# Kernel optimization log

Measured on AMD Instinct MI355X. Metric: run time of the kernel, lower is better.

## Reference

```python
import jax, jax.numpy as jnp
import numpy as np
from jax import lax

H = 512  # LSTM hidden size per direction


def lstm_dir(x, mask, Wih, Whh, bias, reverse):
    # x: [B,L,D], mask: [B,L] float. Masked update follows VarMaskedFastLSTM:
    # state = state_prev + (state_new - state_prev) * mask[t]
    B = x.shape[0]
    h0 = jnp.zeros((B, H), x.dtype)
    c0 = jnp.zeros((B, H), x.dtype)
    xs = jnp.swapaxes(x, 0, 1)      # [L,B,D]
    ms = jnp.swapaxes(mask, 0, 1)   # [L,B]
    if reverse:
        xs, ms = xs[::-1], ms[::-1]
    gx = jnp.einsum('lbd,gd->lbg', xs, Wih) + bias  # precompute input projection [L,B,4H]

    def step(carry, inp):
        h, c = carry
        g_in, mt = inp
        gates = g_in + h @ Whh.T
        i, f, g, o = jnp.split(gates, 4, axis=-1)  # torch gate order i,f,g,o
        c_new = jax.nn.sigmoid(f) * c + jax.nn.sigmoid(i) * jnp.tanh(g)
        h_new = jax.nn.sigmoid(o) * jnp.tanh(c_new)
        m = mt[:, None]
        h = h + (h_new - h) * m
        c = c + (c_new - c) * m
        return (h, c), h

    _, hs = lax.scan(step, (h0, c0), (gx, ms))
    if reverse:
        hs = hs[::-1]
    return jnp.swapaxes(hs, 0, 1)  # [B,L,H]


def bilstm(x, mask, w_ih0, w_hh0, b0, w_ih, w_hh, b):
    out = jnp.concatenate([
        lstm_dir(x, mask, w_ih0[0], w_hh0[0], b0[0], False),
        lstm_dir(x, mask, w_ih0[1], w_hh0[1], b0[1], True)], axis=-1)
    for l in range(2):  # layers 1,2 take 2H-dim input
        out = jnp.concatenate([
            lstm_dir(out, mask, w_ih[l, 0], w_hh[l, 0], b[l, 0], False),
            lstm_dir(out, mask, w_ih[l, 1], w_hh[l, 1], b[l, 1], True)], axis=-1)
    return out  # [B,L,2H]


def setup_inputs() -> dict:
    key = jax.random.key(0)
    ks = jax.random.split(key, 16)
    B, L = 32, 128
    Vin, Vout, E = 32000, 32000, 128
    s = 0.04  # ~1/sqrt(H) init scale
    inp = {}
    inp['inp_word'] = jax.random.randint(ks[0], (B, L), 0, Vin)
    inp['inp_mask'] = jnp.ones((B, L), jnp.float32)
    inp['pri_mask'] = jax.random.randint(ks[1], (B, L), 0, 2).astype(bool)
    inp['tgt_word'] = jax.random.randint(ks[2], (B, L), 0, Vout)
    inp['emb'] = jax.random.normal(ks[3], (Vin, E), jnp.float32) * s
    inp['w_ih0'] = jax.random.normal(ks[4], (2, 4 * H, E), jnp.float32) * s
    inp['w_hh0'] = jax.random.normal(ks[5], (2, 4 * H, H), jnp.float32) * s
    inp['b0'] = jax.random.normal(ks[6], (2, 4 * H), jnp.float32) * s
    inp['w_ih'] = jax.random.normal(ks[7], (2, 2, 4 * H, 2 * H), jnp.float32) * s
    inp['w_hh'] = jax.random.normal(ks[8], (2, 2, 4 * H, H), jnp.float32) * s
    inp['b'] = jax.random.normal(ks[9], (2, 2, 4 * H), jnp.float32) * s
    inp['dec_w1'] = jax.random.normal(ks[10], (128, 2 * H), jnp.float32) * s
    inp['dec_b1'] = jnp.zeros((128,), jnp.float32)
    inp['dec_w2'] = jax.random.normal(ks[11], (Vout, 128), jnp.float32) * s
    inp['dec_b2'] = jnp.zeros((Vout,), jnp.float32)
    inp['ce_weight'] = jax.random.uniform(ks[12], (Vout,), jnp.float32, 0.5, 1.5)
    return inp


def reference(inp_word, inp_mask, pri_mask, tgt_word, emb, w_ih0, w_hh0, b0,
              w_ih, w_hh, b, dec_w1, dec_b1, dec_w2, dec_b2, ce_weight):
    x = emb[inp_word]  # [B,L,E]; inp_drop is identity in eval mode
    seq = bilstm(x, inp_mask, w_ih0, w_hh0, b0, w_ih, w_hh, b)  # [B,L,1024]
    hid = jax.nn.relu(jnp.einsum('blh,dh->bld', seq, dec_w1) + dec_b1)
    decoded = jax.nn.log_softmax(jnp.einsum('bld,vd->blv', hid, dec_w2) + dec_b2, axis=-1)
    rcv_word = jnp.argmax(decoded, axis=-1)
    # Faithful to original: F.cross_entropy applies log_softmax again on the
    # already log-softmaxed decoder output, with class weights (weighted mean).
    lp = jax.nn.log_softmax(decoded, axis=-1)
    B, L, V = lp.shape
    lp = lp.reshape(B * L, V)
    tgt = tgt_word.reshape(-1)
    w = ce_weight[tgt]
    nll = -jnp.take_along_axis(lp, tgt[:, None], axis=1)[:, 0]
    loss = jnp.sum(nll * w) / jnp.sum(w)
    return loss, rcv_word
```

## Files before the change

### kernel.cpp

```cpp
#include <hip/hip_runtime.h>
#include <math.h>

#define Lq 128
#define Bq 32
#define Hq 512
#define VOC 32000

__global__ __launch_bounds__(256) void embed_k(const int* __restrict__ word,
                                               const float* __restrict__ emb,
                                               float* __restrict__ x_tm) {
  int r = blockIdx.x * 2 + (threadIdx.x >> 7);
  int e = threadIdx.x & 127;
  int t = r >> 5, b = r & 31;
  int w = word[b * Lq + t];
  x_tm[(size_t)r * 128 + e] = emb[(size_t)w * 128 + e];
}

__global__ __launch_bounds__(256) void gemm_k(const float* __restrict__ A,
                                              const float* __restrict__ W,
                                              const float* __restrict__ bias,
                                              float* __restrict__ C,
                                              int N, int K, int relu) {
  __shared__ float As[32][132];
  __shared__ float Ws[32][132];
  int tid = threadIdx.x;
  int tx = tid & 15, ty = tid >> 4;
  int rb = blockIdx.y * 128, cb = blockIdx.x * 128;
  float acc[8][8];
#pragma unroll
  for (int i = 0; i < 8; ++i)
#pragma unroll
    for (int j = 0; j < 8; ++j) acc[i][j] = 0.f;

  for (int k0 = 0; k0 < K; k0 += 32) {
#pragma unroll
    for (int j = 0; j < 4; ++j) {
      int f = tid + 256 * j;
      int r = f >> 3, kq = (f & 7) * 4;
      float4 va = *(const float4*)&A[(size_t)(rb + r) * K + k0 + kq];
      As[kq + 0][r] = va.x; As[kq + 1][r] = va.y; As[kq + 2][r] = va.z; As[kq + 3][r] = va.w;
      float4 vw = *(const float4*)&W[(size_t)(cb + r) * K + k0 + kq];
      Ws[kq + 0][r] = vw.x; Ws[kq + 1][r] = vw.y; Ws[kq + 2][r] = vw.z; Ws[kq + 3][r] = vw.w;
    }
    __syncthreads();
#pragma unroll 8
    for (int kk = 0; kk < 32; ++kk) {
      float a[8], w[8];
      *(float4*)&a[0] = *(const float4*)&As[kk][ty * 8];
      *(float4*)&a[4] = *(const float4*)&As[kk][ty * 8 + 4];
      *(float4*)&w[0] = *(const float4*)&Ws[kk][tx * 8];
      *(float4*)&w[4] = *(const float4*)&Ws[kk][tx * 8 + 4];
#pragma unroll
      for (int i = 0; i < 8; ++i)
#pragma unroll
        for (int j = 0; j < 8; ++j)
          acc[i][j] = fmaf(a[i], w[j], acc[i][j]);
    }
    __syncthreads();
  }
#pragma unroll
  for (int i = 0; i < 8; ++i) {
    int r = rb + ty * 8 + i;
#pragma unroll
    for (int j = 0; j < 8; j += 4) {
      int c = cb + tx * 8 + j;
      float4 o;
      o.x = acc[i][j + 0] + bias[c + 0];
      o.y = acc[i][j + 1] + bias[c + 1];
      o.z = acc[i][j + 2] + bias[c + 2];
      o.w = acc[i][j + 3] + bias[c + 3];
      if (relu) {
        o.x = fmaxf(o.x, 0.f); o.y = fmaxf(o.y, 0.f);
        o.z = fmaxf(o.z, 0.f); o.w = fmaxf(o.w, 0.f);
      }
      *(float4*)&C[(size_t)r * N + c] = o;
    }
  }
}

__global__ __launch_bounds__(256) void lstm_step_k(
    const float* __restrict__ GX, const float* __restrict__ Whh,
    const float* __restrict__ mask, const float* __restrict__ Hprev,
    float* __restrict__ Hnext, float* __restrict__ Cst,
    float* __restrict__ seq_out, int s) {
  __shared__ float h_s[32][513];
  __shared__ float w_s[16][513];
  __shared__ float red[8][32][16];
  __shared__ float gate2[32][16];
  int tid = threadIdx.x;
  int d = blockIdx.x >> 7;
  int hcB = (blockIdx.x & 127) * 4;
  int t = d ? (Lq - 1 - s) : s;
  const float* Hd = Hprev + d * (Bq * Hq);
  float* Hn = Hnext + d * (Bq * Hq);
  float* Cd = Cst + d * (Bq * Hq);

#pragma unroll
  for (int j = 0; j < 16; ++j) {
    int f = tid + 256 * j;
    int b = f >> 7, k4 = (f & 127) * 4;
    float4 v = *(const float4*)&Hd[b * 512 + k4];
    h_s[b][k4 + 0] = v.x; h_s[b][k4 + 1] = v.y; h_s[b][k4 + 2] = v.z; h_s[b][k4 + 3] = v.w;
  }
#pragma unroll
  for (int j = 0; j < 8; ++j) {
    int f = tid + 256 * j;
    int c = f >> 7, k4 = (f & 127) * 4;
    int grow = d * 2048 + (c >> 2) * 512 + hcB + (c & 3);
    float4 v = *(const float4*)&Whh[(size_t)grow * 512 + k4];
    w_s[c][k4 + 0] = v.x; w_s[c][k4 + 1] = v.y; w_s[c][k4 + 2] = v.z; w_s[c][k4 + 3] = v.w;
  }
  __syncthreads();

  int tile = tid & 31, ks = tid >> 5;
  int b0 = (tile & 7) * 4, c0 = (tile >> 3) * 4;
  float acc[4][4];
#pragma unroll
  for (int i = 0; i < 4; ++i)
#pragma unroll
    for (int j = 0; j < 4; ++j) acc[i][j] = 0.f;
  int kb = ks * 64;
#pragma unroll 4
  for (int k = kb; k < kb + 64; ++k) {
    float hv[4], wv[4];
    hv[0] = h_s[b0 + 0][k]; hv[1] = h_s[b0 + 1][k];
    hv[2] = h_s[b0 + 2][k]; hv[3] = h_s[b0 + 3][k];
    wv[0] = w_s[c0 + 0][k]; wv[1] = w_s[c0 + 1][k];
    wv[2] = w_s[c0 + 2][k]; wv[3] = w_s[c0 + 3][k];
#pragma unroll
    for (int i = 0; i < 4; ++i)
#pragma unroll
      for (int j = 0; j < 4; ++j)
        acc[i][j] = fmaf(hv[i], wv[j], acc[i][j]);
  }
#pragma unroll
  for (int i = 0; i < 4; ++i)
#pragma unroll
    for (int j = 0; j < 4; ++j) red[ks][b0 + i][c0 + j] = acc[i][j];
  __syncthreads();

  for (int o = tid; o < 512; o += 256) {
    int b = o >> 4, c = o & 15;
    float g = 0.f;
#pragma unroll
    for (int q = 0; q < 8; ++q) g += red[q][b][c];
    g += GX[(size_t)(t * 32 + b) * 4096 + d * 2048 + (c >> 2) * 512 + hcB + (c & 3)];
    gate2[b][c] = g;
  }
  __syncthreads();

  if (tid < 128) {
    int b = tid >> 2, hcl = tid & 3;
    int hh = hcB + hcl;
    float iv = gate2[b][0 + hcl], fv = gate2[b][4 + hcl];
    float gv = gate2[b][8 + hcl], ov = gate2[b][12 + hcl];
    float cp = Cd[b * 512 + hh];
    float hp = h_s[b][hh];
    float m = mask[b * Lq + t];
    float ig = 1.f / (1.f + expf(-iv));
    float fg = 1.f / (1.f + expf(-fv));
    float gg = tanhf(gv);
    float og = 1.f / (1.f + expf(-ov));
    float cn = fg * cp + ig * gg;
    float hn = og * tanhf(cn);
    float ho = hp + (hn - hp) * m;
    float co = cp + (cn - cp) * m;
    Cd[b * 512 + hh] = co;
    Hn[b * 512 + hh] = ho;
    seq_out[(size_t)(t * 32 + b) * 1024 + d * 512 + hh] = ho;
  }
}

__global__ __launch_bounds__(256) void dec_k(
    const float* __restrict__ hid, const float* __restrict__ w2,
    const float* __restrict__ b2, const int* __restrict__ tgt_word,
    float* __restrict__ part) {
  __shared__ float ht[128][68];
  __shared__ float wt[128][68];
  __shared__ float lg[64][68];
  int tid = threadIdx.x;
  int vb = blockIdx.x, rb = blockIdx.y;
  int r0 = rb * 64, v0 = vb * 512;
#pragma unroll
  for (int j = 0; j < 8; ++j) {
    int f = tid + 256 * j;
    int r = f >> 5, kq = (f & 31) * 4;
    float4 v = *(const float4*)&hid[(size_t)(r0 + r) * 128 + kq];
    ht[kq + 0][r] = v.x; ht[kq + 1][r] = v.y; ht[kq + 2][r] = v.z; ht[kq + 3][r] = v.w;
  }
  float M = -INFINITY, S = 0.f, Tl = 0.f;
  int Iv = 0, tgtv = -1;
  if (tid < 64) {
    int r = r0 + tid, t = r >> 5, b = r & 31;
    tgtv = tgt_word[b * Lq + t];
  }
  int nvt = min(8, (VOC - v0 + 63) >> 6);
  int tx = tid & 15, ty = tid >> 4;
  for (int vt = 0; vt < nvt; ++vt) {
    int vbase = v0 + vt * 64;
    __syncthreads();
#pragma unroll
    for (int j = 0; j < 8; ++j) {
      int f = tid + 256 * j;
      int v = f >> 5, kq = (f & 31) * 4;
      int vg = vbase + v;
      float4 x = make_float4(0.f, 0.f, 0.f, 0.f);
      if (vg < VOC) x = *(const float4*)&w2[(size_t)vg * 128 + kq];
      wt[kq + 0][v] = x.x; wt[kq + 1][v] = x.y; wt[kq + 2][v] = x.z; wt[kq + 3][v] = x.w;
    }
    __syncthreads();
    float acc[4][4];
#pragma unroll
    for (int i = 0; i < 4; ++i)
#pragma unroll
      for (int j = 0; j < 4; ++j) acc[i][j] = 0.f;
#pragma unroll 4
    for (int k = 0; k < 128; ++k) {
      float a[4], w[4];
      *(float4*)a = *(const float4*)&ht[k][ty * 4];
      *(float4*)w = *(const float4*)&wt[k][tx * 4];
#pragma unroll
      for (int i = 0; i < 4; ++i)
#pragma unroll
        for (int j = 0; j < 4; ++j)
          acc[i][j] = fmaf(a[i], w[j], acc[i][j]);
    }
#pragma unroll
    for (int i = 0; i < 4; ++i)
#pragma unroll
      for (int j = 0; j < 4; ++j) {
        int v = vbase + tx * 4 + j;
        lg[ty * 4 + i][tx * 4 + j] = acc[i][j] + (v < VOC ? b2[v] : 0.f);
      }
    __syncthreads();
    if (tid < 64) {
      for (int j = 0; j < 64; ++j) {
        int v = vbase + j;
        if (v >= VOC) break;
        float val = lg[tid][j];
        if (val > M) { S = S * expf(M - val) + 1.f; M = val; Iv = v; }
        else S += expf(val - M);
        if (v == tgtv) Tl = val;
      }
    }
  }
  if (tid < 64) {
    int r = r0 + tid;
    float4 o; o.x = M; o.y = S; o.z = (float)Iv; o.w = Tl;
    *(float4*)&part[((size_t)vb * 4096 + r) * 4] = o;
  }
}

__global__ __launch_bounds__(256) void dec_fin_k(
    const float* __restrict__ part, const int* __restrict__ tgt_word,
    const float* __restrict__ cew, float* __restrict__ out,
    float* __restrict__ rowred) {
  int r = blockIdx.x * 256 + threadIdx.x;
  float M = -INFINITY, S = 0.f, If = 0.f;
  for (int ch = 0; ch < 63; ++ch) {
    float4 p = *(const float4*)&part[((size_t)ch * 4096 + r) * 4];
    if (p.x > M) { S = S * expf(M - p.x) + p.y; M = p.x; If = p.z; }
    else S += p.y * expf(p.x - M);
  }
  int t = r >> 5, b = r & 31;
  int tgt = tgt_word[b * Lq + t];
  float Tl = part[((size_t)(tgt >> 9) * 4096 + r) * 4 + 3];
  float lse = M + logf(S);
  float w = cew[tgt];
  out[1 + b * Lq + t] = If;
  rowred[r] = (lse - Tl) * w;
  rowred[4096 + r] = w;
}

__global__ __launch_bounds__(256) void loss_k(const float* __restrict__ rowred,
                                              float* __restrict__ out) {
  __shared__ float s1[256], s2[256];
  float a = 0.f, c = 0.f;
  for (int r = threadIdx.x; r < 4096; r += 256) { a += rowred[r]; c += rowred[4096 + r]; }
  s1[threadIdx.x] = a; s2[threadIdx.x] = c;
  __syncthreads();
  for (int o = 128; o > 0; o >>= 1) {
    if ((int)threadIdx.x < o) { s1[threadIdx.x] += s1[threadIdx.x + o]; s2[threadIdx.x] += s2[threadIdx.x + o]; }
    __syncthreads();
  }
  if (threadIdx.x == 0) out[0] = s1[0] / s2[0];
}

extern "C" void kernel_launch(void* const* d_in, const int* in_sizes, int n_in,
                              void* d_out, int out_size, void* d_ws, size_t ws_size,
                              hipStream_t stream) {
  (void)in_sizes; (void)n_in; (void)out_size; (void)ws_size;
  const int*   inp_word = (const int*)d_in[0];
  const float* inp_mask = (const float*)d_in[1];
  const int*   tgt_word = (const int*)d_in[3];
  const float* emb      = (const float*)d_in[4];
  const float* w_ih0    = (const float*)d_in[5];
  const float* w_hh0    = (const float*)d_in[6];
  const float* b0       = (const float*)d_in[7];
  const float* w_ih     = (const float*)d_in[8];
  const float* w_hh     = (const float*)d_in[9];
  const float* bb       = (const float*)d_in[10];
  const float* dec_w1   = (const float*)d_in[11];
  const float* dec_b1   = (const float*)d_in[12];
  const float* dec_w2   = (const float*)d_in[13];
  const float* dec_b2   = (const float*)d_in[14];
  const float* cew      = (const float*)d_in[15];
  float* out = (float*)d_out;
  float* ws  = (float*)d_ws;

  float* x_tm   = ws;
  float* seqA   = x_tm + 524288;
  float* seqB   = seqA + 4194304;
  float* GX     = seqB + 4194304;
  float* hid    = GX + 16777216;
  float* Hst    = hid + 524288;
  float* Cst    = Hst + 65536;
  float* part   = Cst + 32768;
  float* rowred = part + 1032192;

  embed_k<<<2048, 256, 0, stream>>>(inp_word, emb, x_tm);

  gemm_k<<<dim3(32, 32), 256, 0, stream>>>(x_tm, w_ih0, b0, GX, 4096, 128, 0);
  hipMemsetAsync(Hst, 0, (65536 + 32768) * sizeof(float), stream);
  for (int s = 0; s < 128; ++s)
    lstm_step_k<<<256, 256, 0, stream>>>(GX, w_hh0, inp_mask,
        Hst + (s & 1) * 32768, Hst + ((s & 1) ^ 1) * 32768, Cst, seqA, s);

  gemm_k<<<dim3(32, 32), 256, 0, stream>>>(seqA, w_ih, bb, GX, 4096, 1024, 0);
  hipMemsetAsync(Hst, 0, (65536 + 32768) * sizeof(float), stream);
  for (int s = 0; s < 128; ++s)
    lstm_step_k<<<256, 256, 0, stream>>>(GX, w_hh, inp_mask,
        Hst + (s & 1) * 32768, Hst + ((s & 1) ^ 1) * 32768, Cst, seqB, s);

  gemm_k<<<dim3(32, 32), 256, 0, stream>>>(seqB, w_ih + (size_t)2 * 2048 * 1024,
                                           bb + 4096, GX, 4096, 1024, 0);
  hipMemsetAsync(Hst, 0, (65536 + 32768) * sizeof(float), stream);
  for (int s = 0; s < 128; ++s)
    lstm_step_k<<<256, 256, 0, stream>>>(GX, w_hh + (size_t)2 * 2048 * 512, inp_mask,
        Hst + (s & 1) * 32768, Hst + ((s & 1) ^ 1) * 32768, Cst, seqA, s);

  gemm_k<<<dim3(1, 32), 256, 0, stream>>>(seqA, dec_w1, dec_b1, hid, 128, 1024, 1);
  dec_k<<<dim3(63, 64), 256, 0, stream>>>(hid, dec_w2, dec_b2, tgt_word, part);
  dec_fin_k<<<16, 256, 0, stream>>>(part, tgt_word, cew, out, rowred);
  loss_k<<<1, 256, 0, stream>>>(rowred, out);
}
```

Before: 6.961 ms.

## Replace per-timestep LSTM launches with persistent kernel using global flag barriers

The 384 per-timestep LSTM kernel launches (128 per layer) become one persistent kernel per layer. Its 256 workgroups keep their slice of Whh resident in LDS for all timesteps, keep the cell state in a register, and synchronise across timesteps by spinning on per-workgroup flags in global memory. The aim is to remove launch overhead and the repeated reload of Whh and cell state from global memory at every step. In exchange it relies on all 256 workgroups being co-resident (one per CU with about 136KB of LDS each). The spin loop has a bounded timeout that could silently continue without synchronising, and the flags are read with relaxed ordering.

```diff
diff --git a/kernel.cpp b/kernel.cpp
--- a/kernel.cpp
+++ b/kernel.cpp
@@ -5,6 +5,8 @@
 #define Bq 32
 #define Hq 512
 #define VOC 32000
+
+typedef float f32x4 __attribute__((ext_vector_type(4)));
 
 __global__ __launch_bounds__(256) void embed_k(const int* __restrict__ word,
                                                const float* __restrict__ emb,
@@ -78,96 +80,134 @@
   }
 }
 
-__global__ __launch_bounds__(256) void lstm_step_k(
+#define HSP 516
+#define LSTM_DYN_LDS 136064
+
+__global__ __launch_bounds__(256, 1) void lstm_persist(
     const float* __restrict__ GX, const float* __restrict__ Whh,
-    const float* __restrict__ mask, const float* __restrict__ Hprev,
-    float* __restrict__ Hnext, float* __restrict__ Cst,
-    float* __restrict__ seq_out, int s) {
-  __shared__ float h_s[32][513];
-  __shared__ float w_s[16][513];
-  __shared__ float red[8][32][16];
-  __shared__ float gate2[32][16];
+    const float* __restrict__ mask, float* Hst,
+    float* __restrict__ seq_out, int* flags, int layer) {
+  extern __shared__ float smem[];
+  float* h_s = smem;
+  float* w_s = h_s + 32 * HSP;
+  float* red = w_s + 16 * HSP;
+  float* g2  = red + 8704;
+
   int tid = threadIdx.x;
-  int d = blockIdx.x >> 7;
-  int hcB = (blockIdx.x & 127) * 4;
-  int t = d ? (Lq - 1 - s) : s;
-  const float* Hd = Hprev + d * (Bq * Hq);
-  float* Hn = Hnext + d * (Bq * Hq);
-  float* Cd = Cst + d * (Bq * Hq);
-
-#pragma unroll
-  for (int j = 0; j < 16; ++j) {
-    int f = tid + 256 * j;
-    int b = f >> 7, k4 = (f & 127) * 4;
-    float4 v = *(const float4*)&Hd[b * 512 + k4];
-    h_s[b][k4 + 0] = v.x; h_s[b][k4 + 1] = v.y; h_s[b][k4 + 2] = v.z; h_s[b][k4 + 3] = v.w;
-  }
+  int wg = blockIdx.x;
+  int d = wg >> 7;
+  int hcB = (wg & 127) * 4;
+  int base = layer * 128;
+
+  int ks = tid & 15;
+  int tile = tid >> 4;
+  int q = tile & 7;
+  int c0 = (tile >> 3) * 8;
+
 #pragma unroll
   for (int j = 0; j < 8; ++j) {
     int f = tid + 256 * j;
     int c = f >> 7, k4 = (f & 127) * 4;
     int grow = d * 2048 + (c >> 2) * 512 + hcB + (c & 3);
-    float4 v = *(const float4*)&Whh[(size_t)grow * 512 + k4];
-    w_s[c][k4 + 0] = v.x; w_s[c][k4 + 1] = v.y; w_s[c][k4 + 2] = v.z; w_s[c][k4 + 3] = v.w;
-  }
-  __syncthreads();
-
-  int tile = tid & 31, ks = tid >> 5;
-  int b0 = (tile & 7) * 4, c0 = (tile >> 3) * 4;
-  float acc[4][4];
-#pragma unroll
-  for (int i = 0; i < 4; ++i)
-#pragma unroll
-    for (int j = 0; j < 4; ++j) acc[i][j] = 0.f;
-  int kb = ks * 64;
-#pragma unroll 4
-  for (int k = kb; k < kb + 64; ++k) {
-    float hv[4], wv[4];
-    hv[0] = h_s[b0 + 0][k]; hv[1] = h_s[b0 + 1][k];
-    hv[2] = h_s[b0 + 2][k]; hv[3] = h_s[b0 + 3][k];
-    wv[0] = w_s[c0 + 0][k]; wv[1] = w_s[c0 + 1][k];
-    wv[2] = w_s[c0 + 2][k]; wv[3] = w_s[c0 + 3][k];
-#pragma unroll
-    for (int i = 0; i < 4; ++i)
-#pragma unroll
-      for (int j = 0; j < 4; ++j)
-        acc[i][j] = fmaf(hv[i], wv[j], acc[i][j]);
-  }
-#pragma unroll
-  for (int i = 0; i < 4; ++i)
-#pragma unroll
-    for (int j = 0; j < 4; ++j) red[ks][b0 + i][c0 + j] = acc[i][j];
-  __syncthreads();
-
-  for (int o = tid; o < 512; o += 256) {
-    int b = o >> 4, c = o & 15;
-    float g = 0.f;
-#pragma unroll
-    for (int q = 0; q < 8; ++q) g += red[q][b][c];
-    g += GX[(size_t)(t * 32 + b) * 4096 + d * 2048 + (c >> 2) * 512 + hcB + (c & 3)];
-    gate2[b][c] = g;
-  }
-  __syncthreads();
-
-  if (tid < 128) {
-    int b = tid >> 2, hcl = tid & 3;
-    int hh = hcB + hcl;
-    float iv = gate2[b][0 + hcl], fv = gate2[b][4 + hcl];
-    float gv = gate2[b][8 + hcl], ov = gate2[b][12 + hcl];
-    float cp = Cd[b * 512 + hh];
-    float hp = h_s[b][hh];
-    float m = mask[b * Lq + t];
-    float ig = 1.f / (1.f + expf(-iv));
-    float fg = 1.f / (1.f + expf(-fv));
-    float gg = tanhf(gv);
-    float og = 1.f / (1.f + expf(-ov));
-    float cn = fg * cp + ig * gg;
-    float hn = og * tanhf(cn);
-    float ho = hp + (hn - hp) * m;
-    float co = cp + (cn - cp) * m;
-    Cd[b * 512 + hh] = co;
-    Hn[b * 512 + hh] = ho;
-    seq_out[(size_t)(t * 32 + b) * 1024 + d * 512 + hh] = ho;
+    f32x4 v = *(const f32x4*)&Whh[(size_t)grow * 512 + k4];
+    *(f32x4*)&w_s[c * HSP + k4] = v;
+  }
+
+  float creg = 0.f;
+
+  for (int t = 0; t < 128; ++t) {
+    int tdata = d ? (127 - t) : t;
+    if (t > 0) {
+      int tgt = base + t;
+      int spin = 0;
+      while (__hip_atomic_load(&flags[tid], __ATOMIC_RELAXED,
+                               __HIP_MEMORY_SCOPE_AGENT) < tgt) {
+        if (++spin > 2000000) break;
+        __builtin_amdgcn_s_sleep(2);
+      }
+    }
+    __syncthreads();
+
+    {
+      const float* Hprev = Hst + (t & 1) * 32768 + d * 16384;
+#pragma unroll 16
+      for (int j = 0; j < 64; ++j) {
+        int f = tid + 256 * j;
+        int b = f >> 9, k = f & 511;
+        float v = 0.f;
+        if (t > 0)
+          v = __hip_atomic_load(Hprev + b * 512 + k, __ATOMIC_RELAXED,
+                                __HIP_MEMORY_SCOPE_AGENT);
+        h_s[b * HSP + k] = v;
+      }
+    }
+    __syncthreads();
+
+    float acc[4][8];
+#pragma unroll
+    for (int m = 0; m < 4; ++m)
+#pragma unroll
+      for (int c = 0; c < 8; ++c) acc[m][c] = 0.f;
+#pragma unroll
+    for (int j = 0; j < 8; ++j) {
+      int k0 = 4 * ks + 64 * j;
+      f32x4 hv[4], wvv[8];
+#pragma unroll
+      for (int m = 0; m < 4; ++m) hv[m] = *(const f32x4*)&h_s[(q + 8 * m) * HSP + k0];
+#pragma unroll
+      for (int c = 0; c < 8; ++c) wvv[c] = *(const f32x4*)&w_s[(c0 + c) * HSP + k0];
+#pragma unroll
+      for (int m = 0; m < 4; ++m)
+#pragma unroll
+        for (int c = 0; c < 8; ++c)
+#pragma unroll
+          for (int kk = 0; kk < 4; ++kk)
+            acc[m][c] = fmaf(hv[m][kk], wvv[c][kk], acc[m][c]);
+    }
+#pragma unroll
+    for (int m = 0; m < 4; ++m)
+#pragma unroll
+      for (int c = 0; c < 8; ++c)
+        red[(q + 8 * m) * 272 + (c0 + c) * 17 + ks] = acc[m][c];
+    __syncthreads();
+
+#pragma unroll
+    for (int rep = 0; rep < 2; ++rep) {
+      int o = tid + 256 * rep;
+      int b = o >> 4, c = o & 15;
+      float s = 0.f;
+#pragma unroll
+      for (int kq = 0; kq < 16; ++kq) s += red[b * 272 + c * 17 + kq];
+      s += GX[(size_t)(tdata * 32 + b) * 4096 + d * 2048 + (c >> 2) * 512 + hcB + (c & 3)];
+      g2[b * 17 + c] = s;
+    }
+    __syncthreads();
+
+    if (tid < 128) {
+      int b = tid >> 2, hcl = tid & 3;
+      int hh = hcB + hcl;
+      float iv = g2[b * 17 + 0 + hcl], fv = g2[b * 17 + 4 + hcl];
+      float gv = g2[b * 17 + 8 + hcl], ov = g2[b * 17 + 12 + hcl];
+      float cp = creg;
+      float hp = h_s[b * HSP + hh];
+      float m = mask[b * Lq + tdata];
+      float ig = 1.f / (1.f + expf(-iv));
+      float fg = 1.f / (1.f + expf(-fv));
+      float gg = tanhf(gv);
+      float og = 1.f / (1.f + expf(-ov));
+      float cn = fg * cp + ig * gg;
+      float hn = og * tanhf(cn);
+      float ho = hp + (hn - hp) * m;
+      creg = cp + (cn - cp) * m;
+      float* Hnext = Hst + ((t + 1) & 1) * 32768 + d * 16384;
+      __hip_atomic_store(Hnext + b * 512 + hh, ho, __ATOMIC_RELAXED,
+                         __HIP_MEMORY_SCOPE_AGENT);
+      seq_out[(size_t)(tdata * 32 + b) * 1024 + d * 512 + hh] = ho;
+    }
+    __syncthreads();
+    if (tid == 0)
+      __hip_atomic_store(&flags[wg], base + t + 1, __ATOMIC_RELAXED,
+                         __HIP_MEMORY_SCOPE_AGENT);
   }
 }
 
@@ -317,27 +357,24 @@
   float* Cst    = Hst + 65536;
   float* part   = Cst + 32768;
   float* rowred = part + 1032192;
-
+  int*   flags  = (int*)(rowred + 8192);
+
+  hipFuncSetAttribute((const void*)lstm_persist,
+                      hipFuncAttributeMaxDynamicSharedMemorySize, LSTM_DYN_LDS);
+
+  hipMemsetAsync(flags, 0, 256 * sizeof(int), stream);
   embed_k<<<2048, 256, 0, stream>>>(inp_word, emb, x_tm);
 
   gemm_k<<<dim3(32, 32), 256, 0, stream>>>(x_tm, w_ih0, b0, GX, 4096, 128, 0);
-  hipMemsetAsync(Hst, 0, (65536 + 32768) * sizeof(float), stream);
-  for (int s = 0; s < 128; ++s)
-    lstm_step_k<<<256, 256, 0, stream>>>(GX, w_hh0, inp_mask,
-        Hst + (s & 1) * 32768, Hst + ((s & 1) ^ 1) * 32768, Cst, seqA, s);
+  lstm_persist<<<256, 256, LSTM_DYN_LDS, stream>>>(GX, w_hh0, inp_mask, Hst, seqA, flags, 0);
 
   gemm_k<<<dim3(32, 32), 256, 0, stream>>>(seqA, w_ih, bb, GX, 4096, 1024, 0);
-  hipMemsetAsync(Hst, 0, (65536 + 32768) * sizeof(float), stream);
-  for (int s = 0; s < 128; ++s)
-    lstm_step_k<<<256, 256, 0, stream>>>(GX, w_hh, inp_mask,
-        Hst + (s & 1) * 32768, Hst + ((s & 1) ^ 1) * 32768, Cst, seqB, s);
+  lstm_persist<<<256, 256, LSTM_DYN_LDS, stream>>>(GX, w_hh, inp_mask, Hst, seqB, flags, 1);
 
   gemm_k<<<dim3(32, 32), 256, 0, stream>>>(seqB, w_ih + (size_t)2 * 2048 * 1024,
                                            bb + 4096, GX, 4096, 1024, 0);
-  hipMemsetAsync(Hst, 0, (65536 + 32768) * sizeof(float), stream);
-  for (int s = 0; s < 128; ++s)
-    lstm_step_k<<<256, 256, 0, stream>>>(GX, w_hh + (size_t)2 * 2048 * 512, inp_mask,
-        Hst + (s & 1) * 32768, Hst + ((s & 1) ^ 1) * 32768, Cst, seqA, s);
+  lstm_persist<<<256, 256, LSTM_DYN_LDS, stream>>>(GX, w_hh + (size_t)2 * 2048 * 512,
+                                                   inp_mask, Hst, seqA, flags, 2);
 
   gemm_k<<<dim3(1, 32), 256, 0, stream>>>(seqA, dec_w1, dec_b1, hid, 128, 1024, 1);
   dec_k<<<dim3(63, 64), 256, 0, stream>>>(hid, dec_w2, dec_b2, tgt_word, part);
```

New measurement: 12.52 ms. +79.8%, slower.
